# Optimization experiments

Hardware: AMD Instinct MI355X
Metric: run time of the kernel (lower is better)

The kernel has to match this reference:

```python
import jax, jax.numpy as jnp
import numpy as np

T, N, D, A = 32, 16, 256, 256  # timesteps, batch, vector_dim, cc_acc (vector_dim == cc_acc)
F1, F2 = 512, 256              # feature_dims
TAU_LIF = 2.0
TAU_SDC = 2.0
V_TH = 1.0
ALPHA = 2.0  # ATan surrogate alpha

@jax.custom_vjp
def atan_spike(v):
    # Heaviside(v) with ATan surrogate gradient (v is membrane - threshold)
    return (v >= 0.0).astype(v.dtype)

def _atan_fwd(v):
    return atan_spike(v), v

def _atan_bwd(v, g):
    # d/dv ATan surrogate: (alpha/2) / (1 + (pi/2 * alpha * v)^2); alpha=2 -> 1/(1+(pi v)^2)
    return (g / (1.0 + (jnp.pi * v) ** 2),)

atan_spike.defvjp(_atan_fwd, _atan_bwd)

def lif_scan(x_seq, tau=TAU_LIF, v_th=V_TH):
    # spikingjelly LIFNode: decay_input=True, hard reset to v_reset=0
    def step(v, x):
        v = v + (x - v) / tau
        s = atan_spike(v - v_th)
        return v * (1.0 - s), s
    _, s_seq = jax.lax.scan(step, jnp.zeros_like(x_seq[0]), x_seq)
    return s_seq

def exp_filter(x_seq, decay):
    # y_t = y_{t-1} * decay + x_t
    def step(y, x):
        y = y * decay + x
        return y, y
    _, y_seq = jax.lax.scan(step, jnp.zeros_like(x_seq[0]), x_seq)
    return y_seq


def setup_inputs() -> dict:
    key = jax.random.key(0)
    ks = jax.random.split(key, 8)
    x = jax.random.uniform(ks[0], (T, N, 2, D), dtype=jnp.float32)
    W_sdc = jax.random.normal(ks[1], (2, A), dtype=jnp.float32) / np.sqrt(2.0)
    b_sdc = jnp.zeros((A,), jnp.float32)
    w_syn = jnp.asarray(-np.log(10.0 - 1.0), jnp.float32)  # SynapseFilter tau=10, learnable param
    W_pool = jax.random.normal(ks[2], (A, 1), dtype=jnp.float32) / np.sqrt(A)
    b_pool = jnp.zeros((1,), jnp.float32)
    W_f1 = jax.random.normal(ks[3], (A, F1), dtype=jnp.float32) / np.sqrt(A)
    b_f1 = jnp.zeros((F1,), jnp.float32)
    W_f2 = jax.random.normal(ks[4], (F1, F2), dtype=jnp.float32) / np.sqrt(F1)
    b_f2 = jnp.zeros((F2,), jnp.float32)
    W_out = jax.random.normal(ks[5], (F2, 1), dtype=jnp.float32) / np.sqrt(F2)
    b_out = jnp.zeros((1,), jnp.float32)
    return {"x": x, "W_sdc": W_sdc, "b_sdc": b_sdc, "w_syn": w_syn,
            "W_pool": W_pool, "b_pool": b_pool, "W_f1": W_f1, "b_f1": b_f1,
            "W_f2": W_f2, "b_f2": b_f2, "W_out": W_out, "b_out": b_out}


def reference(x, W_sdc, b_sdc, w_syn, W_pool, b_pool, W_f1, b_f1, W_f2, b_f2, W_out, b_out):
    # TransposeLayer((2,3)): [T,N,2,D] -> [T,N,D,2]
    xt = jnp.swapaxes(x, 2, 3)
    # SDCLinear(cc_acc, tau=2): Linear 2->A with exponential synaptic-current dynamics
    h = jnp.einsum('tndi,ia->tnda', xt, W_sdc) + b_sdc
    i_seq = exp_filter(h, 1.0 - 1.0 / TAU_SDC)          # [T,N,D,A]
    s1 = lif_scan(i_seq)                                 # LIF neuron, tau=2
    syn = exp_filter(s1, 1.0 - jax.nn.sigmoid(w_syn))    # SynapseFilter tau=10 (learnable)
    z = (jnp.einsum('tnda,ao->tndo', syn, W_pool) + b_pool)[..., 0]  # Linear(A,1)+Flatten -> [T,N,D]
    s2 = lif_scan(z)
    # MLP head: Linear(A,F1)+LIF, Linear(F1,F2)+LIF (D == A)
    h1 = lif_scan(jnp.einsum('tnd,df->tnf', s2, W_f1) + b_f1)
    h2 = lif_scan(jnp.einsum('tnf,fg->tng', h1, W_f2) + b_f2)
    o = jnp.einsum('tng,go->tno', h2, W_out) + b_out     # [T,N,1]
    # NonSpikingIFNode: v_t = v_{t-1} + o_t (membrane readout, no spikes)
    return jnp.cumsum(o, axis=0)
```

## Files before the change

### kernel.cpp

```cpp
#include <hip/hip_runtime.h>

#define T_ 32
#define N_ 16
#define D_ 256
#define A_ 256
#define F1_ 512
#define F2_ 256
#define M_ (T_ * N_)
#define FS_ 16
#define GS_ 16

__global__ __launch_bounds__(64) void k1_sdc(const float* __restrict__ x,
    const float* __restrict__ Wsdc, const float* __restrict__ bsdc,
    const float* __restrict__ wsyn, const float* __restrict__ Wpool,
    const float* __restrict__ bpool, float* __restrict__ s2) {
  const int blk = blockIdx.x;
  const int n = blk >> 8;
  const int d = blk & 255;
  const int lane = threadIdx.x;

  const float syn_decay = 1.0f - 1.0f / (1.0f + expf(-wsyn[0]));
  const float bp = bpool[0];

  const int tl = lane >> 1, il = lane & 1;
  const float xv = x[(((tl * N_ + n) * 2) + il) * D_ + d];

  float w0[4], w1[4], ba[4], wp[4], cur[4], vm[4], syn[4];
#pragma unroll
  for (int j = 0; j < 4; ++j) {
    const int a = lane + 64 * j;
    w0[j] = Wsdc[a];
    w1[j] = Wsdc[A_ + a];
    ba[j] = bsdc[a];
    wp[j] = Wpool[a];
    cur[j] = 0.0f; vm[j] = 0.0f; syn[j] = 0.0f;
  }
  float v2 = 0.0f;

  for (int t = 0; t < T_; ++t) {
    const float x0 = __shfl(xv, 2 * t, 64);
    const float x1 = __shfl(xv, 2 * t + 1, 64);
    float c = 0.0f;
#pragma unroll
    for (int j = 0; j < 4; ++j) {
      const float h = x0 * w0[j] + x1 * w1[j] + ba[j];
      cur[j] = cur[j] * 0.5f + h;
      float v = vm[j] + (cur[j] - vm[j]) * 0.5f;
      const bool sp = (v >= 1.0f);
      syn[j] = syn[j] * syn_decay + (sp ? 1.0f : 0.0f);
      vm[j] = sp ? 0.0f : v;
      c += syn[j] * wp[j];
    }
#pragma unroll
    for (int m = 1; m < 64; m <<= 1) c += __shfl_xor(c, m, 64);
    const float z = c + bp;
    v2 = v2 + (z - v2) * 0.5f;
    const bool sp2 = (v2 >= 1.0f);
    if (lane == 0) s2[(t * N_ + n) * D_ + d] = sp2 ? 1.0f : 0.0f;
    v2 = sp2 ? 0.0f : v2;
  }
}

__global__ __launch_bounds__(256) void kA_gemm1(const float* __restrict__ s2,
    const float* __restrict__ Wf1, const float* __restrict__ bf1,
    float* __restrict__ h1, float* __restrict__ partial, int* __restrict__ cnt) {
  __shared__ __align__(16) float s2l[T_ * 260];
  __shared__ __align__(16) float g1l[T_ * FS_];
  const int bx = blockIdx.x;
  const int n = bx >> 5, fs = bx & 31;
  const int tid = threadIdx.x;

  if (bx == 0) {
    partial[tid] = 0.0f;
    partial[tid + 256] = 0.0f;
    if (tid < N_) cnt[tid] = 0;
  }

  {
    const float4* g4 = (const float4*)s2;
    float4* l4 = (float4*)s2l;
#pragma unroll
    for (int r = 0; r < 8; ++r) {
      const int i4 = r * 256 + tid;
      const int t = i4 >> 6, dq = i4 & 63;
      l4[t * 65 + dq] = g4[(t * N_ + n) * 64 + dq];
    }
  }
  __syncthreads();

  const int f = tid & 15, tg = tid >> 4;
  const float* wc = Wf1 + fs * FS_ + f;
  float acc[2][4] = {};
#pragma unroll
  for (int kc = 0; kc < 4; ++kc) {
#pragma unroll 4
    for (int d0 = kc * 64; d0 < kc * 64 + 64; d0 += 4) {
      const float w0 = wc[(d0 + 0) * F1_], w1 = wc[(d0 + 1) * F1_],
                  w2 = wc[(d0 + 2) * F1_], w3 = wc[(d0 + 3) * F1_];
#pragma unroll
      for (int j = 0; j < 2; ++j) {
        const float4 sv = *(const float4*)&s2l[(tg * 2 + j) * 260 + d0];
        acc[j][kc] += sv.x * w0; acc[j][kc] += sv.y * w1;
        acc[j][kc] += sv.z * w2; acc[j][kc] += sv.w * w3;
      }
    }
  }
  const float b = bf1[fs * FS_ + f];
#pragma unroll
  for (int j = 0; j < 2; ++j) {
    float g = b;
    g += acc[j][0]; g += acc[j][1]; g += acc[j][2]; g += acc[j][3];
    g1l[(tg * 2 + j) * FS_ + f] = g;
  }
  __syncthreads();

  if (tid < FS_) {
    float v = 0.0f;
#pragma unroll
    for (int t = 0; t < T_; ++t) {
      const float g = g1l[t * FS_ + tid];
      v = v + (g - v) * 0.5f;
      const bool sp = (v >= 1.0f);
      h1[(t * N_ + n) * F1_ + fs * FS_ + tid] = sp ? 1.0f : 0.0f;
      v = sp ? 0.0f : v;
    }
  }
}

__global__ __launch_bounds__(256) void kB_gemm2(const float* __restrict__ h1,
    const float* __restrict__ Wf2, const float* __restrict__ bf2,
    const float* __restrict__ Wout, const float* __restrict__ bout,
    float* __restrict__ partial, int* __restrict__ cnt, float* __restrict__ out) {
  __shared__ __align__(16) float h1l[T_ * 516];
  __shared__ __align__(16) float g2l[T_ * GS_];
  __shared__ __align__(16) float h2l[T_ * GS_];
  __shared__ int lastFlag;
  const int bx = blockIdx.x;
  const int n = bx >> 4, gs = bx & 15;
  const int tid = threadIdx.x;

  {
    const float4* g4 = (const float4*)h1;
    float4* l4 = (float4*)h1l;
#pragma unroll
    for (int r = 0; r < 16; ++r) {
      const int i4 = r * 256 + tid;
      const int t = i4 >> 7, fq = i4 & 127;
      l4[t * 129 + fq] = g4[(t * N_ + n) * 128 + fq];
    }
  }
  __syncthreads();

  const int g = tid & 15, tg = tid >> 4;
  const float* wc = Wf2 + gs * GS_ + g;
  float acc[2][8] = {};
#pragma unroll
  for (int kc = 0; kc < 8; ++kc) {
#pragma unroll 4
    for (int d0 = kc * 64; d0 < kc * 64 + 64; d0 += 4) {
      const float w0 = wc[(d0 + 0) * F2_], w1 = wc[(d0 + 1) * F2_],
                  w2 = wc[(d0 + 2) * F2_], w3 = wc[(d0 + 3) * F2_];
#pragma unroll
      for (int j = 0; j < 2; ++j) {
        const float4 hv = *(const float4*)&h1l[(tg * 2 + j) * 516 + d0];
        acc[j][kc] += hv.x * w0; acc[j][kc] += hv.y * w1;
        acc[j][kc] += hv.z * w2; acc[j][kc] += hv.w * w3;
      }
    }
  }
  const float b = bf2[gs * GS_ + g];
#pragma unroll
  for (int j = 0; j < 2; ++j) {
    float z = b;
#pragma unroll
    for (int kc = 0; kc < 8; ++kc) z += acc[j][kc];
    g2l[(tg * 2 + j) * GS_ + g] = z;
  }
  __syncthreads();

  if (tid < GS_) {
    float v = 0.0f;
#pragma unroll
    for (int t = 0; t < T_; ++t) {
      const float gv = g2l[t * GS_ + tid];
      v = v + (gv - v) * 0.5f;
      const bool sp = (v >= 1.0f);
      h2l[t * GS_ + tid] = sp ? 1.0f : 0.0f;
      v = sp ? 0.0f : v;
    }
  }
  __syncthreads();

  if (tid < T_) {
    float pp = 0.0f;
#pragma unroll
    for (int j2 = 0; j2 < GS_; ++j2)
      pp += h2l[tid * GS_ + j2] * Wout[gs * GS_ + j2];
    __hip_atomic_fetch_add(&partial[tid * N_ + n], pp,
                           __ATOMIC_RELAXED, __HIP_MEMORY_SCOPE_AGENT);
  }
  __syncthreads();

  if (tid == 0) {
    __threadfence();
    const int old = __hip_atomic_fetch_add(&cnt[n], 1,
                        __ATOMIC_ACQ_REL, __HIP_MEMORY_SCOPE_AGENT);
    lastFlag = (old == 15);
  }
  __syncthreads();

  if (lastFlag && tid < T_) {
    float val = __hip_atomic_load(&partial[tid * N_ + n],
                    __ATOMIC_RELAXED, __HIP_MEMORY_SCOPE_AGENT) + bout[0];
#pragma unroll
    for (int off = 1; off < 32; off <<= 1) {
      const float up = __shfl_up(val, off, 64);
      if (tid >= off) val += up;
    }
    out[tid * N_ + n] = val;
  }
}

extern "C" void kernel_launch(void* const* d_in, const int* in_sizes, int n_in,
                              void* d_out, int out_size, void* d_ws, size_t ws_size,
                              hipStream_t stream) {
  (void)in_sizes; (void)n_in; (void)out_size; (void)ws_size;
  const float* x     = (const float*)d_in[0];
  const float* Wsdc  = (const float*)d_in[1];
  const float* bsdc  = (const float*)d_in[2];
  const float* wsyn  = (const float*)d_in[3];
  const float* Wpool = (const float*)d_in[4];
  const float* bpool = (const float*)d_in[5];
  const float* Wf1   = (const float*)d_in[6];
  const float* bf1   = (const float*)d_in[7];
  const float* Wf2   = (const float*)d_in[8];
  const float* bf2   = (const float*)d_in[9];
  const float* Wout  = (const float*)d_in[10];
  const float* bout  = (const float*)d_in[11];
  float* out = (float*)d_out;

  float* s2      = (float*)d_ws;
  float* h1      = s2 + M_ * D_;
  float* partial = h1 + M_ * F1_;
  int*   cnt     = (int*)(partial + T_ * N_);

  hipLaunchKernelGGL(k1_sdc, dim3(N_ * D_), dim3(64), 0, stream,
                     x, Wsdc, bsdc, wsyn, Wpool, bpool, s2);
  hipLaunchKernelGGL(kA_gemm1, dim3(N_ * (F1_ / FS_)), dim3(256), 0, stream,
                     s2, Wf1, bf1, h1, partial, cnt);
  hipLaunchKernelGGL(kB_gemm2, dim3(N_ * (F2_ / GS_)), dim3(256), 0, stream,
                     h1, Wf2, bf2, Wout, bout, partial, cnt, out);
}
```

Measured before the change: 51.28 us.

## Pack SDC/LIF math into float2 vectors, batch s2 stores, split GEMM2 finer

The first kernel's per-neuron recurrences are rewritten on two-wide float vectors so the compiler can emit packed FP32 ops. x is now read directly per timestep instead of being broadcast through shuffles. The spike output is gathered in registers and written once at the end by 32 lanes, instead of one lane storing on every step. GEMM2 now uses 8 output columns per block instead of 16, doubling its block count to 512 for more parallelism, at the cost of each block reloading the full h1 tile into shared memory.

New measurement: 60.40 us. +17.8%, slower.

```diff
diff --git a/kernel.cpp b/kernel.cpp
--- a/kernel.cpp
+++ b/kernel.cpp
@@ -8,7 +8,9 @@
 #define F2_ 256
 #define M_ (T_ * N_)
 #define FS_ 16
-#define GS_ 16
+#define GS_ 8
+
+typedef float v2f __attribute__((ext_vector_type(2)));
 
 __global__ __launch_bounds__(64) void k1_sdc(const float* __restrict__ x,
     const float* __restrict__ Wsdc, const float* __restrict__ bsdc,
@@ -22,43 +24,59 @@
   const float syn_decay = 1.0f - 1.0f / (1.0f + expf(-wsyn[0]));
   const float bp = bpool[0];
 
-  const int tl = lane >> 1, il = lane & 1;
-  const float xv = x[(((tl * N_ + n) * 2) + il) * D_ + d];
-
-  float w0[4], w1[4], ba[4], wp[4], cur[4], vm[4], syn[4];
-#pragma unroll
-  for (int j = 0; j < 4; ++j) {
-    const int a = lane + 64 * j;
-    w0[j] = Wsdc[a];
-    w1[j] = Wsdc[A_ + a];
-    ba[j] = bsdc[a];
-    wp[j] = Wpool[a];
-    cur[j] = 0.0f; vm[j] = 0.0f; syn[j] = 0.0f;
-  }
+  v2f w0a, w0b, w1a, w1b, baa, bab, wpa, wpb;
+  w0a.x = Wsdc[lane];        w0a.y = Wsdc[lane + 64];
+  w0b.x = Wsdc[lane + 128];  w0b.y = Wsdc[lane + 192];
+  w1a.x = Wsdc[A_ + lane];       w1a.y = Wsdc[A_ + lane + 64];
+  w1b.x = Wsdc[A_ + lane + 128]; w1b.y = Wsdc[A_ + lane + 192];
+  baa.x = bsdc[lane];        baa.y = bsdc[lane + 64];
+  bab.x = bsdc[lane + 128];  bab.y = bsdc[lane + 192];
+  wpa.x = Wpool[lane];       wpa.y = Wpool[lane + 64];
+  wpb.x = Wpool[lane + 128]; wpb.y = Wpool[lane + 192];
+
+  v2f cura = {0.f, 0.f}, curb = {0.f, 0.f};
+  v2f vma  = {0.f, 0.f}, vmb  = {0.f, 0.f};
+  v2f syna = {0.f, 0.f}, synb = {0.f, 0.f};
+  v2f sdv; sdv.x = syn_decay; sdv.y = syn_decay;
   float v2 = 0.0f;
-
+  float s2v = 0.0f;
+
+#pragma unroll 8
   for (int t = 0; t < T_; ++t) {
-    const float x0 = __shfl(xv, 2 * t, 64);
-    const float x1 = __shfl(xv, 2 * t + 1, 64);
+    const float x0 = x[((t * N_ + n) * 2 + 0) * D_ + d];
+    const float x1 = x[((t * N_ + n) * 2 + 1) * D_ + d];
+
+    v2f ha = x0 * w0a + x1 * w1a + baa;
+    v2f hb = x0 * w0b + x1 * w1b + bab;
+    cura = cura * 0.5f + ha;
+    curb = curb * 0.5f + hb;
+    v2f va = vma + (cura - vma) * 0.5f;
+    v2f vb = vmb + (curb - vmb) * 0.5f;
+    const bool sp0 = (va.x >= 1.0f), sp1 = (va.y >= 1.0f);
+    const bool sp2 = (vb.x >= 1.0f), sp3 = (vb.y >= 1.0f);
+    v2f spa, spb;
+    spa.x = sp0 ? 1.0f : 0.0f; spa.y = sp1 ? 1.0f : 0.0f;
+    spb.x = sp2 ? 1.0f : 0.0f; spb.y = sp3 ? 1.0f : 0.0f;
+    syna = syna * sdv + spa;
+    synb = synb * sdv + spb;
+    vma.x = sp0 ? 0.0f : va.x; vma.y = sp1 ? 0.0f : va.y;
+    vmb.x = sp2 ? 0.0f : vb.x; vmb.y = sp3 ? 0.0f : vb.y;
+
     float c = 0.0f;
-#pragma unroll
-    for (int j = 0; j < 4; ++j) {
-      const float h = x0 * w0[j] + x1 * w1[j] + ba[j];
-      cur[j] = cur[j] * 0.5f + h;
-      float v = vm[j] + (cur[j] - vm[j]) * 0.5f;
-      const bool sp = (v >= 1.0f);
-      syn[j] = syn[j] * syn_decay + (sp ? 1.0f : 0.0f);
-      vm[j] = sp ? 0.0f : v;
-      c += syn[j] * wp[j];
-    }
+    c += syna.x * wpa.x;
+    c += syna.y * wpa.y;
+    c += synb.x * wpb.x;
+    c += synb.y * wpb.y;
 #pragma unroll
     for (int m = 1; m < 64; m <<= 1) c += __shfl_xor(c, m, 64);
+
     const float z = c + bp;
     v2 = v2 + (z - v2) * 0.5f;
-    const bool sp2 = (v2 >= 1.0f);
-    if (lane == 0) s2[(t * N_ + n) * D_ + d] = sp2 ? 1.0f : 0.0f;
-    v2 = sp2 ? 0.0f : v2;
-  }
+    const bool spk = (v2 >= 1.0f);
+    s2v = (lane == t) ? (spk ? 1.0f : 0.0f) : s2v;
+    v2 = spk ? 0.0f : v2;
+  }
+  if (lane < T_) s2[(lane * N_ + n) * D_ + d] = s2v;
 }
 
 __global__ __launch_bounds__(256) void kA_gemm1(const float* __restrict__ s2,
@@ -136,7 +154,7 @@
   __shared__ __align__(16) float h2l[T_ * GS_];
   __shared__ int lastFlag;
   const int bx = blockIdx.x;
-  const int n = bx >> 4, gs = bx & 15;
+  const int n = bx >> 5, gs = bx & 31;
   const int tid = threadIdx.x;
 
   {
@@ -151,30 +169,25 @@
   }
   __syncthreads();
 
-  const int g = tid & 15, tg = tid >> 4;
+  const int g = tid & 7, tg = tid >> 3;
   const float* wc = Wf2 + gs * GS_ + g;
-  float acc[2][8] = {};
+  float acc[8] = {};
 #pragma unroll
   for (int kc = 0; kc < 8; ++kc) {
 #pragma unroll 4
     for (int d0 = kc * 64; d0 < kc * 64 + 64; d0 += 4) {
       const float w0 = wc[(d0 + 0) * F2_], w1 = wc[(d0 + 1) * F2_],
                   w2 = wc[(d0 + 2) * F2_], w3 = wc[(d0 + 3) * F2_];
-#pragma unroll
-      for (int j = 0; j < 2; ++j) {
-        const float4 hv = *(const float4*)&h1l[(tg * 2 + j) * 516 + d0];
-        acc[j][kc] += hv.x * w0; acc[j][kc] += hv.y * w1;
-        acc[j][kc] += hv.z * w2; acc[j][kc] += hv.w * w3;
-      }
-    }
-  }
-  const float b = bf2[gs * GS_ + g];
-#pragma unroll
-  for (int j = 0; j < 2; ++j) {
-    float z = b;
-#pragma unroll
-    for (int kc = 0; kc < 8; ++kc) z += acc[j][kc];
-    g2l[(tg * 2 + j) * GS_ + g] = z;
+      const float4 hv = *(const float4*)&h1l[tg * 516 + d0];
+      acc[kc] += hv.x * w0; acc[kc] += hv.y * w1;
+      acc[kc] += hv.z * w2; acc[kc] += hv.w * w3;
+    }
+  }
+  {
+    float z = bf2[gs * GS_ + g];
+#pragma unroll
+    for (int kc = 0; kc < 8; ++kc) z += acc[kc];
+    g2l[tg * GS_ + g] = z;
   }
   __syncthreads();
 
@@ -205,7 +218,7 @@
     __threadfence();
     const int old = __hip_atomic_fetch_add(&cnt[n], 1,
                         __ATOMIC_ACQ_REL, __HIP_MEMORY_SCOPE_AGENT);
-    lastFlag = (old == 15);
+    lastFlag = (old == 31);
   }
   __syncthreads();
 
```
